# Kernel tuning notes

Hardware: AMD Instinct MI355X
Metric: run time of the kernel (lower is better)

## Reference

```python
import jax, jax.numpy as jnp
import numpy as np

# dims
B, L, DM, DS, K, E, DFF, R = 16, 1024, 512, 16, 4, 2, 2048, 32
DI = DM  # expand = 1 -> d_inner == d_model

PARAM_NAMES = ['m_in_w','m_conv_w','m_conv_b','m_xproj_w','m_dt_w','m_dt_b','m_A_log','m_D','m_out_w']


def setup_inputs() -> dict:
    key = jax.random.key(0)
    ks = iter(jax.random.split(key, 32))
    def rn(shape, scale=0.02):
        return jax.random.normal(next(ks), shape, dtype=jnp.float32) * scale
    inp = {
        'x': jax.random.normal(next(ks), (B, L, DM), dtype=jnp.float32),
        # per layer (E) and per direction (2: forward mamba, reversed mamba)
        'm_in_w':   rn((E, 2, 2 * DI, DM)),
        'm_conv_w': rn((E, 2, DI, K), 0.1),
        'm_conv_b': jnp.zeros((E, 2, DI), jnp.float32),
        'm_xproj_w': rn((E, 2, R + 2 * DS, DI)),
        'm_dt_w':   rn((E, 2, DI, R), 0.1),
        'm_dt_b':   jnp.full((E, 2, DI), -4.0, jnp.float32) + rn((E, 2, DI), 0.1),
        'm_A_log':  jnp.log(jnp.broadcast_to(jnp.arange(1, DS + 1, dtype=jnp.float32), (E, 2, DI, DS))),
        'm_D':      jnp.ones((E, 2, DI), jnp.float32),
        'm_out_w':  rn((E, 2, DM, DI)),
        # FFN (1x1 convs == linears) and norms per layer
        'ff_w1': rn((E, DFF, DM)), 'ff_b1': jnp.zeros((E, DFF), jnp.float32),
        'ff_w2': rn((E, DM, DFF)), 'ff_b2': jnp.zeros((E, DM), jnp.float32),
        'ln1_g': jnp.ones((E, DM), jnp.float32), 'ln1_b': jnp.zeros((E, DM), jnp.float32),
        'ln2_g': jnp.ones((E, DM), jnp.float32), 'ln2_b': jnp.zeros((E, DM), jnp.float32),
        'lnf_g': jnp.ones((DM,), jnp.float32),   'lnf_b': jnp.zeros((DM,), jnp.float32),
    }
    return inp


def layer_norm(x, g, b, eps=1e-5):
    mu = x.mean(-1, keepdims=True)
    var = ((x - mu) ** 2).mean(-1, keepdims=True)
    return (x - mu) * jax.lax.rsqrt(var + eps) * g + b


def mamba(x, in_w, conv_w, conv_b, xproj_w, dt_w, dt_b, A_log, Dp, out_w):
    # x: (B, L, DM)
    Bsz, Lseq, _ = x.shape
    xz = x @ in_w.T                       # (B, L, 2*DI)
    xc, z = jnp.split(xz, 2, axis=-1)
    # depthwise causal conv1d (kernel K, left pad K-1, truncate to L)
    xp = jnp.pad(xc, ((0, 0), (K - 1, 0), (0, 0)))
    xc = sum(conv_w[:, k] * xp[:, k:k + Lseq, :] for k in range(K)) + conv_b
    xc = jax.nn.silu(xc)
    dbl = xc @ xproj_w.T                  # (B, L, R + 2*DS)
    dt, Bm, Cm = dbl[..., :R], dbl[..., R:R + DS], dbl[..., R + DS:]
    dt = jax.nn.softplus(dt @ dt_w.T + dt_b)  # (B, L, DI)
    A = -jnp.exp(A_log)                   # (DI, DS)

    def step(h, inputs):
        dt_t, B_t, C_t, x_t = inputs      # (B,DI) (B,DS) (B,DS) (B,DI)
        dA = jnp.exp(dt_t[..., None] * A)             # (B, DI, DS)
        h = dA * h + (dt_t * x_t)[..., None] * B_t[:, None, :]
        y = jnp.einsum('bds,bs->bd', h, C_t)
        return h, y

    xs = (dt.transpose(1, 0, 2), Bm.transpose(1, 0, 2), Cm.transpose(1, 0, 2), xc.transpose(1, 0, 2))
    h0 = jnp.zeros((Bsz, DI, DS), dtype=x.dtype)
    _, ys = jax.lax.scan(step, h0, xs)    # ys: (L, B, DI)
    y = ys.transpose(1, 0, 2) + xc * Dp
    y = y * jax.nn.silu(z)
    return y @ out_w.T                    # (B, L, DM)


def _forward(x, m_in_w, m_conv_w, m_conv_b, m_xproj_w, m_dt_w, m_dt_b, m_A_log, m_D, m_out_w,
             ff_w1, ff_b1, ff_w2, ff_b2, ln1_g, ln1_b, ln2_g, ln2_b, lnf_g, lnf_b):
    packs = (m_in_w, m_conv_w, m_conv_b, m_xproj_w, m_dt_w, m_dt_b, m_A_log, m_D, m_out_w)
    for e in range(E):
        p_fwd = tuple(a[e, 0] for a in packs)
        p_rev = tuple(a[e, 1] for a in packs)
        # bidirectional mamba mixing (second block sees the time-flipped sequence)
        new_x = mamba(x, *p_fwd) + mamba(x[:, ::-1], *p_rev)[:, ::-1]
        x = x + new_x
        xn = layer_norm(x, ln1_g[e], ln1_b[e])
        y = jax.nn.gelu(xn @ ff_w1[e].T + ff_b1[e], approximate=False)
        y = y @ ff_w2[e].T + ff_b2[e]
        x = layer_norm(xn + y, ln2_g[e], ln2_b[e])
    return layer_norm(x, lnf_g, lnf_b)


def reference(x, m_in_w, m_conv_w, m_conv_b, m_xproj_w, m_dt_w, m_dt_b, m_A_log, m_D, m_out_w,
              ff_w1, ff_b1, ff_w2, ff_b2, ln1_g, ln1_b, ln2_g, ln2_b, lnf_g, lnf_b):
    return _forward(x, m_in_w, m_conv_w, m_conv_b, m_xproj_w, m_dt_w, m_dt_b, m_A_log, m_D, m_out_w,
                    ff_w1, ff_b1, ff_w2, ff_b2, ln1_g, ln1_b, ln2_g, ln2_b, lnf_g, lnf_b)
```

## Files before the change

kernel.cpp:

```cpp
#include <hip/hip_runtime.h>
#include <hip/hip_bf16.h>
#include <math.h>

#define DEVI __device__ __forceinline__

namespace {
constexpr int kL   = 1024;
constexpr int kDM  = 512;
constexpr int kDS  = 16;
constexpr int kDFF = 2048;
constexpr int kR   = 32;
constexpr int kDI  = 512;
constexpr int kB   = 16;
constexpr int kM   = kB * kL;
constexpr int kNC  = 32;
constexpr int kCH  = kL / kNC;
}

typedef __attribute__((ext_vector_type(8))) short short8;
typedef __attribute__((ext_vector_type(4))) float f32x4;

DEVI float silu_f(float x)     { return x / (1.f + __expf(-x)); }
DEVI float softplus_f(float x) { return fmaxf(x, 0.f) + log1pf(__expf(-fabsf(x))); }
DEVI float gelu_f(float x)     { return 0.5f * x * (1.f + erff(x * 0.70710678118654752f)); }

DEVI unsigned short f2bf(float f) {
    unsigned int u = __float_as_uint(f);
    return (unsigned short)((u + 0x7fffu + ((u >> 16) & 1u)) >> 16);
}
DEVI float bf2f(unsigned short u) {
    return __uint_as_float(((unsigned int)u) << 16);
}
DEVI uint2 pack4(float4 v) {
    uint2 p;
    p.x = (unsigned int)f2bf(v.x) | ((unsigned int)f2bf(v.y) << 16);
    p.y = (unsigned int)f2bf(v.z) | ((unsigned int)f2bf(v.w) << 16);
    return p;
}

typedef const __attribute__((address_space(1))) unsigned int* gas1;
typedef __attribute__((address_space(3))) unsigned int* las3;
DEVI void gload16(const unsigned short* g, unsigned short* l) {
    __builtin_amdgcn_global_load_lds((gas1)g, (las3)l, 16, 0, 0);
}

struct WCvtArgs { const float* src[6]; unsigned int end[6]; };

__global__ __launch_bounds__(256) void cvt_weights_k(
    WCvtArgs a, unsigned short* __restrict__ dst)
{
    unsigned int i = (blockIdx.x * 256 + threadIdx.x) * 4;
    if (i >= a.end[5]) return;
    int j = 0;
    while (i >= a.end[j]) ++j;
    unsigned int base = j ? a.end[j - 1] : 0;
    float4 v = *(const float4*)&a.src[j][i - base];
    *(uint2*)&dst[i] = pack4(v);
}

__global__ __launch_bounds__(256) void init_x_k(
    const float* __restrict__ x, float* __restrict__ xo,
    unsigned short* __restrict__ xb)
{
    size_t i = (size_t)(blockIdx.x * 256 + threadIdx.x) * 4;
    float4 v = *(const float4*)&x[i];
    *(float4*)&xo[i] = v;
    *(uint2*)&xb[i] = pack4(v);
}

template <int BM, int EPI, typename CT>
__global__ __launch_bounds__(512, 2) void gemm8(
    const unsigned short* __restrict__ A, int lda, size_t zA,
    const unsigned short* __restrict__ W, size_t zW,
    CT* __restrict__ C, int ldc, size_t zC,
    const float* __restrict__ biasb, int zBias,
    const float* __restrict__ add, int Kd)
{
    static_assert(BM == 128 || BM == 256, "");
    constexpr int MF = BM / 32;
    constexpr int AL = BM / 64;
    __shared__ alignas(16) unsigned short As[2][BM * 64];
    __shared__ alignas(16) unsigned short Ws[2][256 * 64];

    const int z = blockIdx.z;
    A += (size_t)z * zA; W += (size_t)z * zW; C += (size_t)z * zC;
    const float* bias = biasb ? biasb + (size_t)z * zBias : nullptr;

    const int gx = gridDim.x;
    int flat = blockIdx.y * gx + blockIdx.x;
    const int total = gx * gridDim.y;
    if ((total & 7) == 0) { int q = total >> 3; flat = (flat & 7) * q + (flat >> 3); }
    const int bx = flat % gx;
    const int by = flat / gx;
    const int row0 = by * BM, col0 = bx * 256;

    const int tid = threadIdx.x, lane = tid & 63, wv = tid >> 6;
    const int wm = wv >> 2, wn = wv & 3;

    f32x4 acc[MF][4];
#pragma unroll
    for (int m = 0; m < MF; ++m)
#pragma unroll
        for (int n = 0; n < 4; ++n) acc[m][n] = (f32x4){0.f, 0.f, 0.f, 0.f};

    const int srow = tid >> 3;
    const int sk   = (((tid & 7) ^ (srow & 7)) * 8);
    const unsigned short* Ag = A + (size_t)(row0 + srow) * lda + sk;
    const unsigned short* Wg = W + (size_t)(col0 + srow) * Kd + sk;
    const int ldso = srow * 64 + (tid & 7) * 8;

    auto stage = [&](int buf, int k0) {
#pragma unroll
        for (int i = 0; i < AL; ++i)
            gload16(Ag + (size_t)(64 * i) * lda + k0, &As[buf][ldso + i * 4096]);
#pragma unroll
        for (int i = 0; i < 4; ++i)
            gload16(Wg + (size_t)(64 * i) * Kd + k0, &Ws[buf][ldso + i * 4096]);
    };

    const int nt = Kd / 64;
    stage(0, 0);
    if (nt > 1) stage(1, 64);

    const int fr = lane & 15;
    const int cb = lane >> 4;

    for (int t = 0; t < nt; ++t) {
        if (t + 1 < nt) {
            if constexpr (BM == 256) asm volatile("s_waitcnt vmcnt(8)" ::: "memory");
            else                     asm volatile("s_waitcnt vmcnt(6)" ::: "memory");
        } else {
            asm volatile("s_waitcnt vmcnt(0)" ::: "memory");
        }
        __builtin_amdgcn_s_barrier();
        __builtin_amdgcn_sched_barrier(0);

        const int cur = t & 1;
        __builtin_amdgcn_s_setprio(1);
#pragma unroll
        for (int kh = 0; kh < 2; ++kh) {
            short8 af[MF], bf[4];
#pragma unroll
            for (int m = 0; m < MF; ++m) {
                int r = wm * (BM / 2) + m * 16 + fr;
                af[m] = *(const short8*)
                    &As[cur][r * 64 + ((((kh << 2) | cb) ^ (r & 7)) << 3)];
            }
#pragma unroll
            for (int n = 0; n < 4; ++n) {
                int r = wn * 64 + n * 16 + fr;
                bf[n] = *(const short8*)
                    &Ws[cur][r * 64 + ((((kh << 2) | cb) ^ (r & 7)) << 3)];
            }
#pragma unroll
            for (int m = 0; m < MF; ++m)
#pragma unroll
                for (int n = 0; n < 4; ++n)
                    acc[m][n] = __builtin_amdgcn_mfma_f32_16x16x32_bf16(
                        af[m], bf[n], acc[m][n], 0, 0, 0);
        }
        __builtin_amdgcn_s_setprio(0);

        __builtin_amdgcn_sched_barrier(0);
        __builtin_amdgcn_s_barrier();
        __builtin_amdgcn_sched_barrier(0);
        if (t + 2 < nt) stage(cur, (t + 2) * 64);
    }

    const int cr = (lane >> 4) * 4;
#pragma unroll
    for (int m = 0; m < MF; ++m) {
#pragma unroll
        for (int n = 0; n < 4; ++n) {
            int cn = col0 + wn * 64 + n * 16 + fr;
#pragma unroll
            for (int r = 0; r < 4; ++r) {
                int rr = row0 + wm * (BM / 2) + m * 16 + cr + r;
                size_t idx = (size_t)rr * ldc + cn;
                float v = acc[m][n][r];
                if constexpr (EPI == 0) {
                    if constexpr (__is_same(CT, unsigned short)) C[idx] = f2bf(v);
                    else C[idx] = v;
                } else if constexpr (EPI == 3) {
                    C[idx] = f2bf(gelu_f(v + bias[cn]));
                } else {
                    C[idx] = v + bias[cn] + add[idx];
                }
            }
        }
    }
}

template <int EPI, int BN, typename CT>
__global__ __launch_bounds__(256) void gemm_bf16(
    const unsigned short* __restrict__ A, int lda, size_t zA,
    const unsigned short* __restrict__ W, size_t zW,
    CT* __restrict__ C, int ldc, size_t zC,
    const float* __restrict__ biasb, int zBias,
    unsigned short* __restrict__ auxb, size_t zAux, int Kd)
{
    static_assert(BN == 64 || BN == 128, "");
    constexpr int NF = BN / 32;
    __shared__ alignas(16) unsigned short As[2][128 * 32];
    __shared__ alignas(16) unsigned short Ws[2][BN * 32];

    const int z = blockIdx.z;
    A += (size_t)z * zA; W += (size_t)z * zW; C += (size_t)z * zC;
    const float* bias = biasb ? biasb + (size_t)z * zBias : nullptr;
    unsigned short* aux = auxb ? auxb + (size_t)z * zAux : nullptr;

    const int gx = gridDim.x;
    int flat = blockIdx.y * gx + blockIdx.x;
    const int total = gx * gridDim.y;
    if ((total & 7) == 0) {
        int q = total >> 3;
        flat = (flat & 7) * q + (flat >> 3);
    }
    const int bx = flat % gx;
    const int by = flat / gx;

    const int tid  = threadIdx.x;
    const int lane = tid & 63;
    const int wv   = tid >> 6;
    const int wm   = wv >> 1;
    const int wn   = wv & 1;
    const int row0 = by * 128;
    const int col0 = bx * BN;

    f32x4 acc[4][NF];
#pragma unroll
    for (int m = 0; m < 4; ++m)
#pragma unroll
        for (int n = 0; n < NF; ++n) acc[m][n] = (f32x4){0.f, 0.f, 0.f, 0.f};

    const int sr  = tid >> 2;
    const int scw = (((tid & 3) ^ ((tid >> 3) & 3)) * 8);
    const unsigned short* Ag = A + (size_t)(row0 + sr) * lda + scw;
    const unsigned short* Wg = W + (size_t)(col0 + sr) * Kd + scw;

    auto stage = [&](int buf, int k0) {
        gload16(Ag + k0, &As[buf][tid * 8]);
        gload16(Ag + (size_t)64 * lda + k0, &As[buf][2048 + tid * 8]);
        gload16(Wg + k0, &Ws[buf][tid * 8]);
        if (BN == 128)
            gload16(Wg + (size_t)64 * Kd + k0, &Ws[buf][2048 + tid * 8]);
    };

    const int nt = Kd / 32;
    stage(0, 0);
    __syncthreads();

    const int fr  = lane & 15;
    const int sw8 = (((lane >> 4) ^ ((fr >> 1) & 3)) * 8);

    int cur = 0;
    for (int t = 0; t < nt; ++t) {
        if (t + 1 < nt) stage(cur ^ 1, (t + 1) * 32);
        short8 af[4], bf[NF];
#pragma unroll
        for (int m = 0; m < 4; ++m)
            af[m] = *(const short8*)&As[cur][(wm * 64 + m * 16 + fr) * 32 + sw8];
#pragma unroll
        for (int n = 0; n < NF; ++n)
            bf[n] = *(const short8*)&Ws[cur][(wn * (BN / 2) + n * 16 + fr) * 32 + sw8];
        __builtin_amdgcn_s_setprio(1);
#pragma unroll
        for (int m = 0; m < 4; ++m)
#pragma unroll
            for (int n = 0; n < NF; ++n)
                acc[m][n] = __builtin_amdgcn_mfma_f32_16x16x32_bf16(
                    af[m], bf[n], acc[m][n], 0, 0, 0);
        __builtin_amdgcn_s_setprio(0);
        __syncthreads();
        cur ^= 1;
    }

    const int cr = (lane >> 4) * 4;
#pragma unroll
    for (int m = 0; m < 4; ++m) {
#pragma unroll
        for (int n = 0; n < NF; ++n) {
            int cn = col0 + wn * (BN / 2) + n * 16 + fr;
#pragma unroll
            for (int r = 0; r < 4; ++r) {
                int rr = row0 + wm * 64 + m * 16 + cr + r;
                size_t idx = (size_t)rr * ldc + cn;
                float v = acc[m][n][r];
                if constexpr (EPI == 1) {
                    float sp = softplus_f(v + bias[cn]);
                    if constexpr (__is_same(CT, unsigned short)) C[idx] = f2bf(sp);
                    else C[idx] = sp;
                } else {
                    C[idx] = v;
                    if (cn < 32) aux[(size_t)rr * 32 + cn] = f2bf(v);
                }
            }
        }
    }
}

__global__ __launch_bounds__(128) void conv_silu_k(
    const unsigned short* __restrict__ xz2, unsigned short* __restrict__ xcb,
    const float* __restrict__ wb, const float* __restrict__ biasb)
{
    const int task = blockIdx.x * 128 + threadIdx.x;
    const int g   = task & 63;
    const int c   = (task >> 6) & 31;
    const int b   = (task >> 11) & 15;
    const int dir = (task >> 15) & 1;
    const int d0  = g * 8;

    const unsigned short* xzd = xz2 + (size_t)dir * 1024 + (size_t)b * kL * 2048 + d0;
    unsigned short* xc = xcb + (size_t)dir * kM * kDI + (size_t)b * kL * kDI + d0;
    const float* w    = wb + (size_t)dir * 2048;
    const float* bias = biasb + (size_t)dir * 512;

    float wk[4][8];
#pragma unroll
    for (int k = 0; k < 4; ++k)
#pragma unroll
        for (int j = 0; j < 8; ++j)
            wk[k][j] = w[(d0 + j) * 4 + (dir ? 3 - k : k)];
    float bs[8];
#pragma unroll
    for (int j = 0; j < 8; ++j) bs[j] = bias[d0 + j];

    const int t0 = c * 32;
    const int rbase = dir ? t0 : t0 - 3;

    auto loadrow = [&](int t, float* o) {
        if (t < 0 || t >= kL) {
#pragma unroll
            for (int j = 0; j < 8; ++j) o[j] = 0.f;
            return;
        }
        uint4 p = *(const uint4*)&xzd[(size_t)t * 2048];
        o[0] = bf2f((unsigned short)(p.x & 0xffff));
        o[1] = bf2f((unsigned short)(p.x >> 16));
        o[2] = bf2f((unsigned short)(p.y & 0xffff));
        o[3] = bf2f((unsigned short)(p.y >> 16));
        o[4] = bf2f((unsigned short)(p.z & 0xffff));
        o[5] = bf2f((unsigned short)(p.z >> 16));
        o[6] = bf2f((unsigned short)(p.w & 0xffff));
        o[7] = bf2f((unsigned short)(p.w >> 16));
    };

    float x0[8], x1[8], x2[8];
    loadrow(rbase + 0, x0);
    loadrow(rbase + 1, x1);
    loadrow(rbase + 2, x2);

#pragma unroll 4
    for (int i = 0; i < 32; ++i) {
        float x3[8];
        loadrow(rbase + 3 + i, x3);
        unsigned short o[8];
#pragma unroll
        for (int j = 0; j < 8; ++j) {
            float v = bs[j];
            v = fmaf(wk[0][j], x0[j], v);
            v = fmaf(wk[1][j], x1[j], v);
            v = fmaf(wk[2][j], x2[j], v);
            v = fmaf(wk[3][j], x3[j], v);
            o[j] = f2bf(silu_f(v));
        }
        *(uint4*)&xc[(size_t)(t0 + i) * kDI] = *(uint4*)o;
#pragma unroll
        for (int j = 0; j < 8; ++j) { x0[j] = x1[j]; x1[j] = x2[j]; x2[j] = x3[j]; }
    }
}

__global__ __launch_bounds__(256) void scan_chunk(
    const unsigned short* __restrict__ dtb2, const unsigned short* __restrict__ xcb2,
    const float* __restrict__ dbl2, const float* __restrict__ A_logb,
    float* __restrict__ S2, float* __restrict__ sdt2)
{
    int dir = blockIdx.y;
    const unsigned short* dtb = dtb2 + (size_t)dir * kM * kDI;
    const unsigned short* xcb = xcb2 + (size_t)dir * kM * kDI;
    const float* dbl = dbl2 + (size_t)dir * kM * 64;
    const float* A_log = A_logb + (size_t)dir * 8192;
    float* S   = S2 + (size_t)dir * (kB * kNC * kDS * kDI);
    float* sdt = sdt2 + (size_t)dir * (kB * kNC * kDI);

    int blk  = blockIdx.x;
    int dblk = blk & 1;
    int c    = (blk >> 1) & (kNC - 1);
    int b    = blk >> 6;
    int d    = dblk * 256 + threadIdx.x;

    const float* al = A_log + d * kDS;
    float A[16];
#pragma unroll
    for (int s = 0; s < 16; ++s) A[s] = -__expf(al[s]);

    float h[16];
#pragma unroll
    for (int s = 0; s < 16; ++s) h[s] = 0.f;
    float sum = 0.f;

#pragma unroll 2
    for (int i = 0; i < kCH; ++i) {
        int p   = c * kCH + i;
        int t   = dir ? (kL - 1 - p) : p;
        int row = b * kL + t;
        float dt = bf2f(dtb[(size_t)row * kDI + d]);
        float xv = bf2f(xcb[(size_t)row * kDI + d]);
        sum += dt;
        float dx = dt * xv;
        const float4* bp = (const float4*)(dbl + (size_t)row * 64 + kR);
        float4 b0 = bp[0], b1 = bp[1], b2 = bp[2], b3 = bp[3];
        float Bv[16] = {b0.x, b0.y, b0.z, b0.w, b1.x, b1.y, b1.z, b1.w,
                        b2.x, b2.y, b2.z, b2.w, b3.x, b3.y, b3.z, b3.w};
#pragma unroll
        for (int s = 0; s < 16; ++s) {
            float q = __expf(dt * A[s]);
            h[s] = fmaf(q, h[s], dx * Bv[s]);
        }
    }
    size_t base = (size_t)(b * kNC + c) * kDS * kDI + d;
#pragma unroll
    for (int s = 0; s < 16; ++s) S[base + s * kDI] = h[s];
    sdt[(size_t)(b * kNC + c) * kDI + d] = sum;
}

__global__ __launch_bounds__(256) void scan_carry(
    float* __restrict__ S2, const float* __restrict__ sdt2,
    const float* __restrict__ A_logb)
{
    int dir = blockIdx.y;
    float* S = S2 + (size_t)dir * (kB * kNC * kDS * kDI);
    const float* sdt = sdt2 + (size_t)dir * (kB * kNC * kDI);
    const float* A_log = A_logb + (size_t)dir * 8192;

    int g = blockIdx.x * 256 + threadIdx.x;
    int d = g & (kDI - 1);
    int s = (g >> 9) & 15;
    int b = g >> 13;

    float A = -__expf(A_log[d * kDS + s]);
    float h = 0.f;
#pragma unroll
    for (int c = 0; c < kNC; ++c) {
        size_t base = ((size_t)(b * kNC + c) * kDS + s) * kDI + d;
        float sv = S[base];
        float sd = sdt[(size_t)(b * kNC + c) * kDI + d];
        S[base] = h;
        h = fmaf(__expf(sd * A), h, sv);
    }
}

__global__ __launch_bounds__(256) void scan_emit(
    const unsigned short* __restrict__ dtb2, const unsigned short* __restrict__ xcb2,
    const float* __restrict__ dbl2, const float* __restrict__ A_logb,
    const float* __restrict__ h0v2, const float* __restrict__ Dpb,
    const unsigned short* __restrict__ xz2, unsigned short* __restrict__ yb2)
{
    int dir = blockIdx.y;
    const unsigned short* dtb = dtb2 + (size_t)dir * kM * kDI;
    const unsigned short* xcb = xcb2 + (size_t)dir * kM * kDI;
    const float* dbl = dbl2 + (size_t)dir * kM * 64;
    const float* A_log = A_logb + (size_t)dir * 8192;
    const float* h0v = h0v2 + (size_t)dir * (kB * kNC * kDS * kDI);
    const float* Dp = Dpb + (size_t)dir * 512;
    const unsigned short* zg = xz2 + (size_t)dir * 1024 + 512;
    unsigned short* yb = yb2 + (size_t)dir * kM * kDI;

    int blk  = blockIdx.x;
    int dblk = blk & 1;
    int c    = (blk >> 1) & (kNC - 1);
    int b    = blk >> 6;
    int d    = dblk * 256 + threadIdx.x;

    const float* al = A_log + d * kDS;
    float A[16];
#pragma unroll
    for (int s = 0; s < 16; ++s) A[s] = -__expf(al[s]);
    float Dd = Dp[d];

    size_t hbase = (size_t)(b * kNC + c) * kDS * kDI + d;
    float h[16];
#pragma unroll
    for (int s = 0; s < 16; ++s) h[s] = h0v[hbase + s * kDI];

#pragma unroll 2
    for (int i = 0; i < kCH; ++i) {
        int p   = c * kCH + i;
        int t   = dir ? (kL - 1 - p) : p;
        int row = b * kL + t;
        float dt = bf2f(dtb[(size_t)row * kDI + d]);
        float xv = bf2f(xcb[(size_t)row * kDI + d]);
        float dx = dt * xv;
        const float4* bp = (const float4*)(dbl + (size_t)row * 64 + kR);
        float4 b0 = bp[0], b1 = bp[1], b2 = bp[2], b3 = bp[3];
        const float4* cp = (const float4*)(dbl + (size_t)row * 64 + kR + kDS);
        float4 c0 = cp[0], c1 = cp[1], c2 = cp[2], c3 = cp[3];
        float Bv[16] = {b0.x, b0.y, b0.z, b0.w, b1.x, b1.y, b1.z, b1.w,
                        b2.x, b2.y, b2.z, b2.w, b3.x, b3.y, b3.z, b3.w};
        float Cv[16] = {c0.x, c0.y, c0.z, c0.w, c1.x, c1.y, c1.z, c1.w,
                        c2.x, c2.y, c2.z, c2.w, c3.x, c3.y, c3.z, c3.w};
        float y = 0.f;
#pragma unroll
        for (int s = 0; s < 16; ++s) {
            float q = __expf(dt * A[s]);
            h[s] = fmaf(q, h[s], dx * Bv[s]);
            y = fmaf(h[s], Cv[s], y);
        }
        y += xv * Dd;
        float z = bf2f(zg[(size_t)row * 2048 + d]);
        yb[(size_t)row * kDI + d] = f2bf(y * silu_f(z));
    }
}

__global__ __launch_bounds__(128) void ln_k(
    const float* __restrict__ in, const float* __restrict__ a0,
    const float* __restrict__ a1,
    const float* __restrict__ g, const float* __restrict__ bb,
    float* __restrict__ out, unsigned short* __restrict__ outbf)
{
    int row = blockIdx.x;
    int tid = threadIdx.x;
    size_t off = (size_t)row * kDM + tid * 4;
    float4 v = *(const float4*)&in[off];
    if (a0) {
        float4 u = *(const float4*)&a0[off];
        float4 w = *(const float4*)&a1[off];
        v.x += u.x + w.x; v.y += u.y + w.y; v.z += u.z + w.z; v.w += u.w + w.w;
    }
    float s1 = v.x + v.y + v.z + v.w;
    float s2 = v.x * v.x + v.y * v.y + v.z * v.z + v.w * v.w;
#pragma unroll
    for (int o = 32; o >= 1; o >>= 1) {
        s1 += __shfl_xor(s1, o);
        s2 += __shfl_xor(s2, o);
    }
    __shared__ float red[4];
    if ((tid & 63) == 0) { red[(tid >> 6) * 2] = s1; red[(tid >> 6) * 2 + 1] = s2; }
    __syncthreads();
    s1 = red[0] + red[2];
    s2 = red[1] + red[3];
    float mu  = s1 * (1.f / kDM);
    float var = s2 * (1.f / kDM) - mu * mu;
    float rs  = rsqrtf(var + 1e-5f);
    int cn = tid * 4;
    float4 gv = *(const float4*)&g[cn];
    float4 bv = *(const float4*)&bb[cn];
    float4 o;
    o.x = (v.x - mu) * rs * gv.x + bv.x;
    o.y = (v.y - mu) * rs * gv.y + bv.y;
    o.z = (v.z - mu) * rs * gv.z + bv.z;
    o.w = (v.w - mu) * rs * gv.w + bv.w;
    *(float4*)&out[off] = o;
    if (outbf)
        *(uint2*)&outbf[off] = pack4(o);
}

extern "C" void kernel_launch(void* const* d_in, const int* in_sizes, int n_in,
                              void* d_out, int out_size, void* d_ws, size_t ws_size,
                              hipStream_t stream)
{
    const float* x_in    = (const float*)d_in[0];
    const float* in_w    = (const float*)d_in[1];
    const float* conv_w  = (const float*)d_in[2];
    const float* conv_b  = (const float*)d_in[3];
    const float* xproj_w = (const float*)d_in[4];
    const float* dt_w    = (const float*)d_in[5];
    const float* dt_b    = (const float*)d_in[6];
    const float* A_log   = (const float*)d_in[7];
    const float* Dp      = (const float*)d_in[8];
    const float* out_w   = (const float*)d_in[9];
    const float* ff_w1   = (const float*)d_in[10];
    const float* ff_b1   = (const float*)d_in[11];
    const float* ff_w2   = (const float*)d_in[12];
    const float* ff_b2   = (const float*)d_in[13];
    const float* ln1_g   = (const float*)d_in[14];
    const float* ln1_b   = (const float*)d_in[15];
    const float* ln2_g   = (const float*)d_in[16];
    const float* ln2_b   = (const float*)d_in[17];
    const float* lnf_g   = (const float*)d_in[18];
    const float* lnf_b   = (const float*)d_in[19];

    float* ws = (float*)d_ws;
    unsigned short* wsb = (unsigned short*)d_ws;

    unsigned short* wb_in  = wsb;
    unsigned short* wb_xp  = wsb + 2097152;
    unsigned short* wb_out = wsb + 2228224;
    unsigned short* wb_f1  = wsb + 3276800;
    unsigned short* wb_f2  = wsb + 5373952;
    unsigned short* wb_dt  = wsb + 7471104;

    constexpr size_t A0 = 3768320;
    unsigned short* xbf  = (unsigned short*)(ws + A0);
    unsigned short* xz2  = (unsigned short*)(ws + A0 + 4194304);
    unsigned short* xcb2 = (unsigned short*)(ws + A0 + 20971520);
    unsigned short* yb2  = (unsigned short*)(ws + A0 + 29360128);
    float*          Sb2  = ws + A0 + 37748736;
    unsigned short* dtb2 = (unsigned short*)(ws + A0 + 46137344);
    float*          dbl2 = ws + A0 + 54525952;
    unsigned short* dtin2= (unsigned short*)(ws + A0 + 56623104);
    float*          sdt2 = ws + A0 + 57147392;
    float*          o2   = ws + A0 + 37748736;
    float*          xn   = ws + A0;
    unsigned short* xnbf = (unsigned short*)(ws + A0 + 8388608);
    unsigned short* Hb   = (unsigned short*)(ws + A0 + 12582912);
    float*          t2   = ws + A0 + 29360128;

    float* xcur = (float*)d_out;
    dim3 thr(256);

    WCvtArgs wa;
    wa.src[0] = in_w;    wa.end[0] = 2097152;
    wa.src[1] = xproj_w; wa.end[1] = 2228224;
    wa.src[2] = out_w;   wa.end[2] = 3276800;
    wa.src[3] = ff_w1;   wa.end[3] = 5373952;
    wa.src[4] = ff_w2;   wa.end[4] = 7471104;
    wa.src[5] = dt_w;    wa.end[5] = 7536640;
    cvt_weights_k<<<dim3(7536640 / 1024), thr, 0, stream>>>(wa, wsb);
    init_x_k<<<dim3(8192), thr, 0, stream>>>(x_in, xcur, xbf);

    for (int e = 0; e < 2; ++e) {
        gemm8<256, 0, unsigned short><<<dim3(8, 64, 1), dim3(512), 0, stream>>>(
            xbf, 512, 0, wb_in + (size_t)e * 1048576, 0, xz2, 2048, 0,
            nullptr, 0, nullptr, 512);
        conv_silu_k<<<dim3(512), dim3(128), 0, stream>>>(
            xz2, xcb2, conv_w + (size_t)e * 4096, conv_b + (size_t)e * 1024);
        gemm_bf16<5, 64, float><<<dim3(1, 128, 2), thr, 0, stream>>>(
            xcb2, 512, (size_t)kM * 512, wb_xp + (size_t)e * 65536, 32768,
            dbl2, 64, (size_t)kM * 64, nullptr, 0, dtin2, (size_t)kM * 32, 512);
        gemm_bf16<1, 128, unsigned short><<<dim3(4, 128, 2), thr, 0, stream>>>(
            dtin2, 32, (size_t)kM * 32, wb_dt + (size_t)e * 32768, 16384,
            dtb2, 512, (size_t)kM * 512, dt_b + (size_t)e * 1024, 512,
            nullptr, 0, 32);
        scan_chunk<<<dim3(kB * kNC * 2, 2), thr, 0, stream>>>(
            dtb2, xcb2, dbl2, A_log + (size_t)e * 16384, Sb2, sdt2);
        scan_carry<<<dim3(512, 2), thr, 0, stream>>>(
            Sb2, sdt2, A_log + (size_t)e * 16384);
        scan_emit<<<dim3(kB * kNC * 2, 2), thr, 0, stream>>>(
            dtb2, xcb2, dbl2, A_log + (size_t)e * 16384, Sb2,
            Dp + (size_t)e * 1024, xz2, yb2);
        gemm8<128, 0, float><<<dim3(2, 128, 2), dim3(512), 0, stream>>>(
            yb2, 512, (size_t)kM * 512, wb_out + (size_t)e * 524288, 262144,
            o2, 512, (size_t)kM * 512, nullptr, 0, nullptr, 512);
        ln_k<<<dim3(kM), dim3(128), 0, stream>>>(
            xcur, o2, o2 + (size_t)kM * 512,
            ln1_g + e * kDM, ln1_b + e * kDM, xn, xnbf);
        gemm8<256, 3, unsigned short><<<dim3(8, 64, 1), dim3(512), 0, stream>>>(
            xnbf, 512, 0, wb_f1 + (size_t)e * 1048576, 0, Hb, 2048, 0,
            ff_b1 + (size_t)e * kDFF, 0, nullptr, 512);
        gemm8<128, 4, float><<<dim3(2, 128, 1), dim3(512), 0, stream>>>(
            Hb, 2048, 0, wb_f2 + (size_t)e * 1048576, 0, t2, 512, 0,
            ff_b2 + (size_t)e * kDM, 0, xn, 2048);
        ln_k<<<dim3(kM), dim3(128), 0, stream>>>(
            t2, nullptr, nullptr, ln2_g + e * kDM, ln2_b + e * kDM, xcur,
            e == 0 ? xbf : nullptr);
    }
    ln_k<<<dim3(kM), dim3(128), 0, stream>>>(
        xcur, nullptr, nullptr, lnf_g, lnf_b, xcur, nullptr);
}
```

Baseline: 971.5 us.

## Split GEMM k-tile into quadrant phases interleaving LDS refills with MFMA

The GEMM main loop now splits each 64-wide k-tile into four quadrant MFMA phases, each separated by a barrier. The global-to-LDS prefetch for tile t+2 is issued piecewise between phases, into the same buffer once the relevant quadrant has been read, instead of after all compute. This aims to overlap global loads with MFMA work and smooth memory issue, like an 8-wave ping-pong schedule. It adds three extra block barriers per k-tile. The vmcnt waits may no longer match the new load grouping, which is a correctness and stall risk.

```diff
diff --git a/kernel.cpp b/kernel.cpp
--- a/kernel.cpp
+++ b/kernel.cpp
@@ -68,6 +68,10 @@
     *(uint2*)&xb[i] = pack4(v);
 }
 
+#define SBAR_PIN do { __builtin_amdgcn_sched_barrier(0); \
+    __builtin_amdgcn_s_barrier(); \
+    __builtin_amdgcn_sched_barrier(0); } while (0)
+
 template <int BM, int EPI, typename CT>
 __global__ __launch_bounds__(512, 2) void gemm8(
     const unsigned short* __restrict__ A, int lda, size_t zA,
@@ -78,7 +82,7 @@
 {
     static_assert(BM == 128 || BM == 256, "");
     constexpr int MF = BM / 32;
-    constexpr int AL = BM / 64;
+    constexpr int MQ = BM / 64;
     __shared__ alignas(16) unsigned short As[2][BM * 64];
     __shared__ alignas(16) unsigned short Ws[2][256 * 64];
 
@@ -103,68 +107,102 @@
 #pragma unroll
         for (int n = 0; n < 4; ++n) acc[m][n] = (f32x4){0.f, 0.f, 0.f, 0.f};
 
-    const int srow = tid >> 3;
-    const int sk   = (((tid & 7) ^ (srow & 7)) * 8);
-    const unsigned short* Ag = A + (size_t)(row0 + srow) * lda + sk;
-    const unsigned short* Wg = W + (size_t)(col0 + srow) * Kd + sk;
-    const int ldso = srow * 64 + (tid & 7) * 8;
-
-    auto stage = [&](int buf, int k0) {
-#pragma unroll
-        for (int i = 0; i < AL; ++i)
-            gload16(Ag + (size_t)(64 * i) * lda + k0, &As[buf][ldso + i * 4096]);
-#pragma unroll
-        for (int i = 0; i < 4; ++i)
-            gload16(Wg + (size_t)(64 * i) * Kd + k0, &Ws[buf][ldso + i * 4096]);
+    const int s8  = tid & 7;
+    const int r6  = tid >> 3;
+    const int rhi = tid >> 8;
+
+    auto stA = [&](int buf, int k0, int row) {
+        gload16(A + (size_t)(row0 + row) * lda + k0 + ((s8 ^ (row & 7)) * 8),
+                &As[buf][row * 64 + s8 * 8]);
+    };
+    auto stB = [&](int buf, int k0, int row) {
+        gload16(W + (size_t)(col0 + row) * Kd + k0 + ((s8 ^ (row & 7)) * 8),
+                &Ws[buf][row * 64 + s8 * 8]);
+    };
+    auto stageA = [&](int buf, int k0, int mg) {
+        if constexpr (BM == 256) {
+            stA(buf, k0, mg * 64 + r6);
+            stA(buf, k0, mg * 64 + 128 + r6);
+        } else {
+            stA(buf, k0, mg * 32 + rhi * 64 + (r6 & 31));
+        }
+    };
+    auto stageB = [&](int buf, int k0, int ng) {
+        stB(buf, k0, ng * 32 + rhi * 64 + (r6 & 31));
+        stB(buf, k0, ng * 32 + (2 + rhi) * 64 + (r6 & 31));
     };
 
     const int nt = Kd / 64;
-    stage(0, 0);
-    if (nt > 1) stage(1, 64);
-
-    const int fr = lane & 15;
-    const int cb = lane >> 4;
+    stageA(0, 0, 0); stageA(0, 0, 1); stageB(0, 0, 0); stageB(0, 0, 1);
+    if (nt > 1) { stageA(1, 64, 0); stageA(1, 64, 1); stageB(1, 64, 0); stageB(1, 64, 1); }
+
+    const int fr = lane & 15, cb = lane >> 4;
+    short8 af0[MQ][2], af1[MQ][2], bf0[2][2], bf1[2][2];
+
+    auto rdA = [&](short8 (*dst)[2], int buf, int mg) {
+#pragma unroll
+        for (int m = 0; m < MQ; ++m)
+#pragma unroll
+            for (int kh = 0; kh < 2; ++kh) {
+                int r = wm * (BM / 2) + mg * (BM / 4) + m * 16 + fr;
+                dst[m][kh] = *(const short8*)
+                    &As[buf][r * 64 + ((((kh << 2) | cb) ^ (r & 7)) << 3)];
+            }
+    };
+    auto rdB = [&](short8 (*dst)[2], int buf, int ng) {
+#pragma unroll
+        for (int n = 0; n < 2; ++n)
+#pragma unroll
+            for (int kh = 0; kh < 2; ++kh) {
+                int r = wn * 64 + ng * 32 + n * 16 + fr;
+                dst[n][kh] = *(const short8*)
+                    &Ws[buf][r * 64 + ((((kh << 2) | cb) ^ (r & 7)) << 3)];
+            }
+    };
+    auto mmq = [&](short8 (*Af)[2], short8 (*Bf)[2], int mg, int ng) {
+        __builtin_amdgcn_s_setprio(1);
+#pragma unroll
+        for (int m = 0; m < MQ; ++m)
+#pragma unroll
+            for (int n = 0; n < 2; ++n)
+#pragma unroll
+                for (int kh = 0; kh < 2; ++kh)
+                    acc[mg * MQ + m][ng * 2 + n] =
+                        __builtin_amdgcn_mfma_f32_16x16x32_bf16(
+                            Af[m][kh], Bf[n][kh],
+                            acc[mg * MQ + m][ng * 2 + n], 0, 0, 0);
+        __builtin_amdgcn_s_setprio(0);
+    };
 
     for (int t = 0; t < nt; ++t) {
+        const int cur = t & 1;
+        const bool pf = (t + 2 < nt);
+        const int k2 = (t + 2) * 64;
+
         if (t + 1 < nt) {
             if constexpr (BM == 256) asm volatile("s_waitcnt vmcnt(8)" ::: "memory");
             else                     asm volatile("s_waitcnt vmcnt(6)" ::: "memory");
         } else {
             asm volatile("s_waitcnt vmcnt(0)" ::: "memory");
         }
-        __builtin_amdgcn_s_barrier();
-        __builtin_amdgcn_sched_barrier(0);
-
-        const int cur = t & 1;
-        __builtin_amdgcn_s_setprio(1);
-#pragma unroll
-        for (int kh = 0; kh < 2; ++kh) {
-            short8 af[MF], bf[4];
-#pragma unroll
-            for (int m = 0; m < MF; ++m) {
-                int r = wm * (BM / 2) + m * 16 + fr;
-                af[m] = *(const short8*)
-                    &As[cur][r * 64 + ((((kh << 2) | cb) ^ (r & 7)) << 3)];
-            }
-#pragma unroll
-            for (int n = 0; n < 4; ++n) {
-                int r = wn * 64 + n * 16 + fr;
-                bf[n] = *(const short8*)
-                    &Ws[cur][r * 64 + ((((kh << 2) | cb) ^ (r & 7)) << 3)];
-            }
-#pragma unroll
-            for (int m = 0; m < MF; ++m)
-#pragma unroll
-                for (int n = 0; n < 4; ++n)
-                    acc[m][n] = __builtin_amdgcn_mfma_f32_16x16x32_bf16(
-                        af[m], bf[n], acc[m][n], 0, 0, 0);
-        }
-        __builtin_amdgcn_s_setprio(0);
-
-        __builtin_amdgcn_sched_barrier(0);
-        __builtin_amdgcn_s_barrier();
-        __builtin_amdgcn_sched_barrier(0);
-        if (t + 2 < nt) stage(cur, (t + 2) * 64);
+        SBAR_PIN;
+
+        rdA(af0, cur, 0); rdB(bf0, cur, 0);
+        mmq(af0, bf0, 0, 0);
+        SBAR_PIN;
+
+        rdA(af1, cur, 1);
+        if (pf) { stageA(cur, k2, 0); stageB(cur, k2, 0); }
+        mmq(af1, bf0, 1, 0);
+        SBAR_PIN;
+
+        rdB(bf1, cur, 1);
+        if (pf) stageA(cur, k2, 1);
+        mmq(af1, bf1, 1, 1);
+        SBAR_PIN;
+
+        if (pf) stageB(cur, k2, 1);
+        mmq(af0, bf1, 0, 1);
     }
 
     const int cr = (lane >> 4) * 4;
```

New measurement: 980.2 us. No clear change (+0.9%).
